# Kernel tuning notes

Hardware: AMD Instinct MI355X
Metric: run time of the kernel (lower is better)

Reference implementation:

```python
import jax, jax.numpy as jnp
import numpy as np

B, S, H = 4, 2048, 2048
E, K = 4, 2
FF = 4 * H  # standard MLP expert expansion


def setup_inputs() -> dict:
    key = jax.random.key(0)
    ks = jax.random.split(key, 5)
    sc = 0.02
    return {
        "hidden_states": jax.random.normal(ks[0], (B, S, H), jnp.float32),
        "w_gate": jax.random.normal(ks[1], (H, E), jnp.float32) * sc,
        "b_gate": jnp.zeros((E,), jnp.float32),
        "w1": jax.random.normal(ks[2], (E, H, FF), jnp.float32) * sc,
        "b1": jnp.zeros((E, FF), jnp.float32),
        "w2": jax.random.normal(ks[3], (E, FF, H), jnp.float32) * sc,
        "b2": jnp.zeros((E, H), jnp.float32),
    }


def reference(hidden_states, w_gate, b_gate, w1, b1, w2, b2):
    # Router: linear gate -> softmax -> top-k, renormalized gate weights
    logits = jnp.einsum("bsh,he->bse", hidden_states, w_gate) + b_gate
    probs = jax.nn.softmax(logits, axis=-1)                       # [B,S,E]
    top_p, top_i = jax.lax.top_k(probs, K)                        # [B,S,K]
    gate_w = top_p / jnp.sum(top_p, axis=-1, keepdims=True)

    # Switch-style load-balancing aux loss
    route = jax.nn.one_hot(top_i, E, dtype=probs.dtype)           # [B,S,K,E]
    frac_tokens = jnp.mean(jnp.sum(route, axis=2) / K, axis=(0, 1))  # [E]
    mean_prob = jnp.mean(probs, axis=(0, 1))                      # [E]
    aux_loss = E * jnp.sum(frac_tokens * mean_prob)

    # Dispatch/combine: small fixed expert count -> loop over experts,
    # dense FFN on all tokens, mask via gate weight (0 for unrouted tokens).
    out = jnp.zeros_like(hidden_states)
    for e in range(E):
        w_e = jnp.sum(gate_w * (top_i == e), axis=-1)             # [B,S]
        h = jax.nn.gelu(jnp.einsum("bsh,hf->bsf", hidden_states, w1[e]) + b1[e])
        y = jnp.einsum("bsf,fh->bsh", h, w2[e]) + b2[e]
        out = out + w_e[..., None] * y
    return out, aux_loss
```

## Files before the change

kernel.cpp:

```cpp
#include <hip/hip_runtime.h>

typedef unsigned short u16;
typedef __attribute__((ext_vector_type(8))) short bf16x8;
typedef __attribute__((ext_vector_type(4))) float f32x4;

#define TOK  8192
#define HD   2048
#define FFD  8192
#define NEXP 4
#define CAPE 4352

__device__ __forceinline__ u16 f2bf(float f){
  unsigned u = __float_as_uint(f);
  u += 0x7fffu + ((u >> 16) & 1u);
  return (u16)(u >> 16);
}

__device__ __forceinline__ float gelu_tanh(float x){
  float u = 0.7978845608028654f * (x + 0.044715f * x * x * x);
  return 0.5f * x * (1.0f + tanhf(u));
}

__device__ __forceinline__ void gload_lds16(const void* g, void* l){
  __builtin_amdgcn_global_load_lds((const __attribute__((address_space(1))) void*)g,
                                   (__attribute__((address_space(3))) void*)l, 16, 0, 0);
}

__device__ __forceinline__ f32x4 mfma_bf16(bf16x8 a, bf16x8 b, f32x4 c){
  asm("v_mfma_f32_16x16x32_bf16 %0, %1, %2, %0" : "+v"(c) : "v"(a), "v"(b));
  return c;
}

__global__ __launch_bounds__(256) void cvt_to_bf16(const float* __restrict__ in,
                                                   u16* __restrict__ out, int n4){
  int i = blockIdx.x * 256 + threadIdx.x;
  if (i >= n4) return;
  float4 v = ((const float4*)in)[i];
  ushort4 o;
  o.x = f2bf(v.x); o.y = f2bf(v.y); o.z = f2bf(v.z); o.w = f2bf(v.w);
  ((ushort4*)out)[i] = o;
}

__global__ __launch_bounds__(256) void transpose_cvt(const float* __restrict__ in,
                                                     u16* __restrict__ out, int R, int C){
  __shared__ u16 t[64][138];
  in  += (size_t)blockIdx.z * R * C;
  out += (size_t)blockIdx.z * R * C;
  const int tx = threadIdx.x & 63;
  const int w  = threadIdx.x >> 6;
  const size_t r0 = (size_t)blockIdx.y * 128;
  const size_t c0 = (size_t)blockIdx.x * 64;
  #pragma unroll
  for (int i = 0; i < 32; i++){
    const int r = w * 32 + i;
    t[tx][r] = f2bf(in[(r0 + r) * C + c0 + tx]);
  }
  __syncthreads();
  #pragma unroll
  for (int j = 0; j < 16; j++){
    const int c = j * 4 + w;
    ushort2 o;
    o.x = t[c][2 * tx];
    o.y = t[c][2 * tx + 1];
    *(ushort2*)(out + (c0 + c) * (size_t)R + r0 + 2 * tx) = o;
  }
}

__global__ __launch_bounds__(256) void router_kernel(
    const float* __restrict__ X, const float* __restrict__ wg, const float* __restrict__ bg,
    float* __restrict__ probs, int* __restrict__ topi, float* __restrict__ gatew){
  int t = blockIdx.x;
  const float* x = X + (size_t)t * HD;
  float a0 = 0.f, a1 = 0.f, a2 = 0.f, a3 = 0.f;
  for (int h = threadIdx.x; h < HD; h += 256){
    float xv = x[h];
    float4 w = ((const float4*)wg)[h];
    a0 += xv * w.x; a1 += xv * w.y; a2 += xv * w.z; a3 += xv * w.w;
  }
  __shared__ float red[4][256];
  red[0][threadIdx.x] = a0; red[1][threadIdx.x] = a1;
  red[2][threadIdx.x] = a2; red[3][threadIdx.x] = a3;
  __syncthreads();
  for (int s = 128; s > 0; s >>= 1){
    if (threadIdx.x < (unsigned)s){
      #pragma unroll
      for (int e = 0; e < 4; e++) red[e][threadIdx.x] += red[e][threadIdx.x + s];
    }
    __syncthreads();
  }
  if (threadIdx.x == 0){
    float l[4], p[4];
    #pragma unroll
    for (int e = 0; e < 4; e++) l[e] = red[e][0] + bg[e];
    float mx = fmaxf(fmaxf(l[0], l[1]), fmaxf(l[2], l[3]));
    float s = 0.f;
    #pragma unroll
    for (int e = 0; e < 4; e++){ p[e] = expf(l[e] - mx); s += p[e]; }
    #pragma unroll
    for (int e = 0; e < 4; e++){ p[e] /= s; probs[t * 4 + e] = p[e]; }
    int e0 = 0;
    for (int e = 1; e < 4; e++) if (p[e] > p[e0]) e0 = e;
    int e1 = -1;
    for (int e = 0; e < 4; e++){ if (e == e0) continue; if (e1 < 0 || p[e] > p[e1]) e1 = e; }
    float g = p[e0] + p[e1];
    topi[t * 2] = e0; topi[t * 2 + 1] = e1;
    #pragma unroll
    for (int e = 0; e < 4; e++)
      gatew[(size_t)e * TOK + t] = (e == e0) ? p[e0] / g : (e == e1) ? p[e1] / g : 0.f;
  }
}

__global__ __launch_bounds__(256) void compact_stage(const int* __restrict__ topi,
                                                     int* __restrict__ stage,
                                                     int* __restrict__ cnum){
  const int c = blockIdx.x, tid = threadIdx.x;
  const int t = c * 256 + tid;
  const int lane = tid & 63, w = tid >> 6;
  const int e0 = topi[t * 2], e1 = topi[t * 2 + 1];
  __shared__ int wcnt[4][4], woff[4][4];
  int pos[4]; bool sel[4];
  #pragma unroll
  for (int e = 0; e < 4; e++){
    sel[e] = (e0 == e) || (e1 == e);
    unsigned long long m = __ballot(sel[e]);
    pos[e] = __popcll(m & ((1ull << lane) - 1ull));
    if (lane == 0) wcnt[e][w] = __popcll(m);
  }
  __syncthreads();
  if (tid < 4){
    int s = 0;
    #pragma unroll
    for (int ww = 0; ww < 4; ww++){ woff[tid][ww] = s; s += wcnt[tid][ww]; }
    cnum[tid * 32 + c] = s;
  }
  __syncthreads();
  #pragma unroll
  for (int e = 0; e < 4; e++)
    if (sel[e]) stage[(e * 32 + c) * 256 + woff[e][w] + pos[e]] = t;
}

__global__ __launch_bounds__(64) void scan_chunks(const int* __restrict__ cnum,
                                                  int* __restrict__ coff,
                                                  int* __restrict__ cnt){
  if (threadIdx.x < 4){
    int e = threadIdx.x, s = 0;
    for (int c = 0; c < 32; c++){ coff[e * 32 + c] = s; s += cnum[e * 32 + c]; }
    cnt[e] = s;
  }
}

__global__ __launch_bounds__(256) void compact_write(const int* __restrict__ stage,
                                                     const int* __restrict__ cnum,
                                                     const int* __restrict__ coff,
                                                     int* __restrict__ lists){
  const int c = blockIdx.x, tid = threadIdx.x;
  #pragma unroll
  for (int e = 0; e < 4; e++){
    const int n = cnum[e * 32 + c];
    if (tid < n)
      lists[e * TOK + coff[e * 32 + c] + tid] = stage[(e * 32 + c) * 256 + tid];
  }
}

__global__ __launch_bounds__(256) void aux_kernel(const float* __restrict__ probs,
                                                  const int* __restrict__ topi,
                                                  float* __restrict__ out_aux){
  __shared__ float sp[4][256];
  __shared__ float sc[4][256];
  float p[4] = {0,0,0,0}, c[4] = {0,0,0,0};
  for (int t = threadIdx.x; t < TOK; t += 256){
    #pragma unroll
    for (int e = 0; e < 4; e++) p[e] += probs[t * 4 + e];
    c[topi[t * 2]]     += 1.f;
    c[topi[t * 2 + 1]] += 1.f;
  }
  #pragma unroll
  for (int e = 0; e < 4; e++){ sp[e][threadIdx.x] = p[e]; sc[e][threadIdx.x] = c[e]; }
  __syncthreads();
  for (int s = 128; s > 0; s >>= 1){
    if (threadIdx.x < (unsigned)s){
      #pragma unroll
      for (int e = 0; e < 4; e++){
        sp[e][threadIdx.x] += sp[e][threadIdx.x + s];
        sc[e][threadIdx.x] += sc[e][threadIdx.x + s];
      }
    }
    __syncthreads();
  }
  if (threadIdx.x == 0){
    float aux = 0.f;
    #pragma unroll
    for (int e = 0; e < 4; e++)
      aux += (sc[e][0] / (float)(TOK * 2)) * (sp[e][0] / (float)TOK);
    *out_aux = 4.f * aux;
  }
}

__global__ __launch_bounds__(256) void gemm1_97(
    const u16* __restrict__ Xb, const u16* __restrict__ BT,
    const int* __restrict__ lists, const int* __restrict__ cnt,
    const float* __restrict__ bias, u16* __restrict__ Hout)
{
  __shared__ __align__(16) u16 As[128 * 64];
  __shared__ __align__(16) u16 Bs[128 * 64];
  const int e = blockIdx.z;
  const int Mv = cnt[e];
  const int* rowidx = lists + (size_t)e * TOK;
  BT   += (size_t)e * (size_t)FFD * HD;
  bias += (size_t)e * FFD;
  Hout += (size_t)e * (size_t)CAPE * FFD;

  const int gx = gridDim.x, gy = gridDim.y;
  const int orig = blockIdx.x + gx * blockIdx.y;
  const int xcd = orig & 7, rank = orig >> 3;
  const int bxl = rank / gy, by = rank % gy;
  const int bx = xcd * (gx >> 3) + bxl;
  const int browg = by * 128;
  if (browg >= Mv) return;
  const size_t bcol = (size_t)bx * 128;

  const int tid = threadIdx.x, lane = tid & 63, w = tid >> 6;
  const int wr = w >> 1, wc = w & 1;
  const int l8 = lane >> 3;
  const int csw  = ((lane & 7) ^ l8) * 8;
  const int sw   = (lane & 7) * 8;
  const int h8   = ((lane >> 4) & 3) * 8;
  const int colk0 = h8 ^ sw, colk1 = (32 + h8) ^ sw;
  const int r16 = lane & 15;

  const u16* bsrc[4]; int bch[4];
  #pragma unroll
  for (int j = 0; j < 4; j++){
    int rb = j * 32 + w * 8;
    bch[j] = rb * 128;
    bsrc[j] = BT + (bcol + rb + l8) * (size_t)HD + csw;
  }
  const u16* asrc[4]; int ach[4];
  #pragma unroll
  for (int q = 0; q < 4; q++){
    int rb = wr * 64 + q * 16 + wc * 8;
    ach[q] = rb * 128;
    int rl = browg + rb + l8;
    if (rl > Mv - 1) rl = Mv - 1;
    asrc[q] = Xb + (size_t)rowidx[rl] * HD + csw;
  }

  f32x4 acc[4][4];
  #pragma unroll
  for (int m = 0; m < 4; m++)
    #pragma unroll
    for (int n = 0; n < 4; n++) acc[m][n] = (f32x4){0.f, 0.f, 0.f, 0.f};
  bf16x8 bC[8];

  const int NT = HD / 64;
  for (int t = 0; t < NT; ++t){
    const size_t ko = (size_t)t * 64;
    __syncthreads();
    #pragma unroll
    for (int j = 0; j < 4; j++) gload_lds16(bsrc[j] + ko, (char*)Bs + bch[j]);
    #pragma unroll
    for (int q = 0; q < 4; q++) gload_lds16(asrc[q] + ko, (char*)As + ach[q]);
    __syncthreads();

    #pragma unroll
    for (int nf = 0; nf < 4; nf++){
      const u16* bp = Bs + (wc * 64 + nf * 16 + r16) * 64;
      bC[nf * 2]     = *(const bf16x8*)(bp + colk0);
      bC[nf * 2 + 1] = *(const bf16x8*)(bp + colk1);
    }
    #pragma unroll
    for (int m = 0; m < 4; m++){
      const u16* ap = As + (wr * 64 + m * 16 + r16) * 64;
      bf16x8 a0 = *(const bf16x8*)(ap + colk0);
      bf16x8 a1 = *(const bf16x8*)(ap + colk1);
      #pragma unroll
      for (int nf = 0; nf < 4; nf++){
        acc[m][nf] = mfma_bf16(a0, bC[nf * 2],     acc[m][nf]);
        acc[m][nf] = mfma_bf16(a1, bC[nf * 2 + 1], acc[m][nf]);
      }
    }
  }

  const int cl = r16, rg = (lane >> 4) * 4;
  const size_t c0 = bcol + wc * 64;
  float bv[4];
  #pragma unroll
  for (int nf = 0; nf < 4; nf++) bv[nf] = bias[c0 + nf * 16 + cl];
  #pragma unroll
  for (int mf = 0; mf < 4; mf++){
    const int rbase = browg + wr * 64 + mf * 16 + rg;
    #pragma unroll
    for (int nf = 0; nf < 4; nf++){
      const size_t col = c0 + nf * 16 + cl;
      #pragma unroll
      for (int j = 0; j < 4; j++){
        u16 hv = f2bf(gelu_tanh(acc[mf][nf][j] + bv[nf]));
        __builtin_nontemporal_store(hv, &Hout[(size_t)(rbase + j) * FFD + col]);
      }
    }
  }
}

template<int ATOMIC>
__global__ __launch_bounds__(512) void gemm2_97(
    const u16* __restrict__ Hb, const u16* __restrict__ BT,
    const int* __restrict__ lists, const int* __restrict__ cnt,
    const float* __restrict__ bias, const float* __restrict__ gate,
    float* __restrict__ Cout)
{
  __shared__ __align__(16) u16 As[256 * 64];
  __shared__ __align__(16) u16 Bs[128 * 64];
  const int e = blockIdx.z;
  const int Mv = cnt[e];
  const int* rowidx = lists + (size_t)e * TOK;
  BT   += (size_t)e * (size_t)HD * FFD;
  bias += (size_t)e * HD;
  Hb   += (size_t)e * (size_t)CAPE * FFD;
  gate += (size_t)e * TOK;

  const int gx = gridDim.x, gy = gridDim.y;
  const int nwg = gx * gy;
  const int orig = blockIdx.x + gx * blockIdx.y;
  const int xcd = orig & 7, rank = orig >> 3;
  const int v = xcd * (nwg >> 3) + rank;
  const int bx = v % gx, by = v / gx;
  const int browg = by * 256;
  if (browg >= Mv) return;
  const size_t bcol = (size_t)bx * 128;

  const int tid = threadIdx.x, lane = tid & 63, w = tid >> 6;
  const int wm = w >> 1, wn = w & 1;
  const int l8 = lane >> 3;
  const int csw  = ((lane & 7) ^ l8) * 8;
  const int sw   = (lane & 7) * 8;
  const int h8   = ((lane >> 4) & 3) * 8;
  const int colk0 = h8 ^ sw, colk1 = (32 + h8) ^ sw;
  const int r16 = lane & 15;

  const u16* bsrc[2]; int bch[2];
  #pragma unroll
  for (int j = 0; j < 2; j++){
    int rb = j * 64 + w * 8;
    bch[j] = rb * 128;
    bsrc[j] = BT + (bcol + rb + l8) * (size_t)FFD + csw;
  }
  const u16* asrc[4]; int ach[4];
  #pragma unroll
  for (int q = 0; q < 4; q++){
    int rb = q * 64 + w * 8;
    ach[q] = rb * 128;
    asrc[q] = Hb + (size_t)(browg + rb + l8) * FFD + csw;
  }

  f32x4 acc[4][4];
  #pragma unroll
  for (int m = 0; m < 4; m++)
    #pragma unroll
    for (int n = 0; n < 4; n++) acc[m][n] = (f32x4){0.f, 0.f, 0.f, 0.f};
  bf16x8 bC[8];

  const int NT = FFD / 64;
  for (int t = 0; t < NT; ++t){
    const size_t ko = (size_t)t * 64;
    __syncthreads();
    #pragma unroll
    for (int j = 0; j < 2; j++) gload_lds16(bsrc[j] + ko, (char*)Bs + bch[j]);
    #pragma unroll
    for (int q = 0; q < 4; q++) gload_lds16(asrc[q] + ko, (char*)As + ach[q]);
    __syncthreads();

    #pragma unroll
    for (int nf = 0; nf < 4; nf++){
      const u16* bp = Bs + (wn * 64 + nf * 16 + r16) * 64;
      bC[nf * 2]     = *(const bf16x8*)(bp + colk0);
      bC[nf * 2 + 1] = *(const bf16x8*)(bp + colk1);
    }
    #pragma unroll
    for (int m = 0; m < 4; m++){
      const u16* ap = As + (wm * 64 + m * 16 + r16) * 64;
      bf16x8 a0 = *(const bf16x8*)(ap + colk0);
      bf16x8 a1 = *(const bf16x8*)(ap + colk1);
      #pragma unroll
      for (int nf = 0; nf < 4; nf++){
        acc[m][nf] = mfma_bf16(a0, bC[nf * 2],     acc[m][nf]);
        acc[m][nf] = mfma_bf16(a1, bC[nf * 2 + 1], acc[m][nf]);
      }
    }
  }

  const int cl = r16, rg = (lane >> 4) * 4;
  const size_t c0 = bcol + wn * 64;
  float bv[4];
  #pragma unroll
  for (int nf = 0; nf < 4; nf++) bv[nf] = bias[c0 + nf * 16 + cl];
  #pragma unroll
  for (int mf = 0; mf < 4; mf++){
    const int rbase = browg + wm * 64 + mf * 16 + rg;
    int   tok[4]; float gv[4];
    #pragma unroll
    for (int j = 0; j < 4; j++){
      const bool ok = (rbase + j) < Mv;
      tok[j] = ok ? rowidx[rbase + j] : -1;
      gv[j]  = ok ? gate[tok[j]] : 0.f;
    }
    #pragma unroll
    for (int nf = 0; nf < 4; nf++){
      const size_t col = c0 + nf * 16 + cl;
      #pragma unroll
      for (int j = 0; j < 4; j++){
        if (tok[j] >= 0){
          const size_t idx = (size_t)tok[j] * HD + col;
          float y = gv[j] * (acc[mf][nf][j] + bv[nf]);
          if (ATOMIC) atomicAdd(Cout + idx, y);
          else        Cout[idx] += y;
        }
      }
    }
  }
}

extern "C" void kernel_launch(void* const* d_in, const int* in_sizes, int n_in,
                              void* d_out, int out_size, void* d_ws, size_t ws_size,
                              hipStream_t stream){
  (void)in_sizes; (void)n_in;
  const float* X  = (const float*)d_in[0];
  const float* wg = (const float*)d_in[1];
  const float* bg = (const float*)d_in[2];
  const float* w1 = (const float*)d_in[3];
  const float* b1 = (const float*)d_in[4];
  const float* w2 = (const float*)d_in[5];
  const float* b2 = (const float*)d_in[6];
  float* out = (float*)d_out;

  char* ws = (char*)d_ws;
  size_t off = 0;
  auto alloc = [&](size_t b) -> char* {
    char* p = ws + off;
    off = (off + b + 255) & ~(size_t)255;
    return p;
  };
  u16*   Xb    = (u16*)  alloc((size_t)TOK * HD * 2);
  float* probs = (float*)alloc((size_t)TOK * 4 * 4);
  int*   topi  = (int*)  alloc((size_t)TOK * 2 * 4);
  float* gatew = (float*)alloc((size_t)NEXP * TOK * 4);
  int*   cnt   = (int*)  alloc((size_t)NEXP * 4);
  int*   lists = (int*)  alloc((size_t)NEXP * TOK * 4);
  int*   stage = (int*)  alloc((size_t)NEXP * 32 * 256 * 4);
  int*   cnum  = (int*)  alloc((size_t)NEXP * 32 * 4);
  int*   coff  = (int*)  alloc((size_t)NEXP * 32 * 4);
  const size_t common = off;

  const size_t w1t_all = (size_t)NEXP * FFD * HD * 2;
  const size_t w2t_all = (size_t)NEXP * HD * FFD * 2;
  const size_t hb_all  = (size_t)NEXP * CAPE * FFD * 2;
  const bool merged = ws_size >= common + w1t_all + w2t_all + hb_all + 1024;

  hipMemsetAsync(out, 0, (size_t)TOK * HD * sizeof(float), stream);

  cvt_to_bf16<<<(TOK * HD / 4 + 255) / 256, 256, 0, stream>>>(X, Xb, TOK * HD / 4);
  router_kernel<<<TOK, 256, 0, stream>>>(X, wg, bg, probs, topi, gatew);
  compact_stage<<<32, 256, 0, stream>>>(topi, stage, cnum);
  scan_chunks<<<1, 64, 0, stream>>>(cnum, coff, cnt);
  compact_write<<<32, 256, 0, stream>>>(stage, cnum, coff, lists);
  aux_kernel<<<1, 256, 0, stream>>>(probs, topi, out + (out_size - 1));

  if (merged){
    u16* W1T = (u16*)alloc(w1t_all);
    u16* W2T = (u16*)alloc(w2t_all);
    u16* Hb  = (u16*)alloc(hb_all);
    transpose_cvt<<<dim3(FFD / 64, HD / 128, NEXP), 256, 0, stream>>>(w1, W1T, HD, FFD);
    transpose_cvt<<<dim3(HD / 64, FFD / 128, NEXP), 256, 0, stream>>>(w2, W2T, FFD, HD);
    gemm1_97<<<dim3(FFD / 128, CAPE / 128, NEXP), 256, 0, stream>>>(
        Xb, W1T, lists, cnt, b1, Hb);
    gemm2_97<1><<<dim3(HD / 128, CAPE / 256, NEXP), 512, 0, stream>>>(
        Hb, W2T, lists, cnt, b2, gatew, out);
  } else {
    u16* W1T = (u16*)alloc((size_t)FFD * HD * 2);
    u16* W2T = (u16*)alloc((size_t)HD * FFD * 2);
    u16* Hb  = (u16*)alloc((size_t)CAPE * FFD * 2);
    for (int e = 0; e < NEXP; ++e){
      transpose_cvt<<<dim3(FFD / 64, HD / 128, 1), 256, 0, stream>>>(
          w1 + (size_t)e * HD * FFD, W1T, HD, FFD);
      transpose_cvt<<<dim3(HD / 64, FFD / 128, 1), 256, 0, stream>>>(
          w2 + (size_t)e * FFD * HD, W2T, FFD, HD);
      gemm1_97<<<dim3(FFD / 128, CAPE / 128, 1), 256, 0, stream>>>(
          Xb, W1T, lists + e * TOK, cnt + e, b1 + (size_t)e * FFD, Hb);
      gemm2_97<0><<<dim3(HD / 128, CAPE / 256, 1), 512, 0, stream>>>(
          Hb, W2T, lists + e * TOK, cnt + e, b2 + (size_t)e * HD,
          gatew + (size_t)e * TOK, out);
    }
  }
}
```

Before: 1.664 ms.

## Pipeline gemm1 with 256x256 double-buffered tiles and fuse bf16 cast into router

Replaces the first expert GEMM with a 512-thread 256x256 tile kernel. It double-buffers LDS and interleaves async global-to-LDS loads with MFMA phases, using explicit vmcnt waits, raw barriers and wave priority hints, so memory latency hides behind compute and the tile gets more reuse. The standalone X-to-bf16 conversion kernel is folded into the router, which already reads X, saving one full pass over the activations. The second GEMM changes from 256-row tiles with 512 threads to 128-row tiles with 256 threads, giving more, smaller blocks. This adds complex hand-scheduled synchronisation and register pressure, and a 256-row tile pads more rows per expert.

```diff
diff --git a/kernel.cpp b/kernel.cpp
--- a/kernel.cpp
+++ b/kernel.cpp
@@ -10,6 +10,9 @@
 #define NEXP 4
 #define CAPE 4352
 
+#define S_BARRIER() asm volatile("s_barrier" ::: "memory")
+#define VMCNT(n)    asm volatile("s_waitcnt vmcnt(" #n ")" ::: "memory")
+
 __device__ __forceinline__ u16 f2bf(float f){
   unsigned u = __float_as_uint(f);
   u += 0x7fffu + ((u >> 16) & 1u);
@@ -29,16 +32,6 @@
 __device__ __forceinline__ f32x4 mfma_bf16(bf16x8 a, bf16x8 b, f32x4 c){
   asm("v_mfma_f32_16x16x32_bf16 %0, %1, %2, %0" : "+v"(c) : "v"(a), "v"(b));
   return c;
-}
-
-__global__ __launch_bounds__(256) void cvt_to_bf16(const float* __restrict__ in,
-                                                   u16* __restrict__ out, int n4){
-  int i = blockIdx.x * 256 + threadIdx.x;
-  if (i >= n4) return;
-  float4 v = ((const float4*)in)[i];
-  ushort4 o;
-  o.x = f2bf(v.x); o.y = f2bf(v.y); o.z = f2bf(v.z); o.w = f2bf(v.w);
-  ((ushort4*)out)[i] = o;
 }
 
 __global__ __launch_bounds__(256) void transpose_cvt(const float* __restrict__ in,
@@ -68,14 +61,26 @@
 
 __global__ __launch_bounds__(256) void router_kernel(
     const float* __restrict__ X, const float* __restrict__ wg, const float* __restrict__ bg,
-    float* __restrict__ probs, int* __restrict__ topi, float* __restrict__ gatew){
+    float* __restrict__ probs, int* __restrict__ topi, float* __restrict__ gatew,
+    u16* __restrict__ Xb){
   int t = blockIdx.x;
-  const float* x = X + (size_t)t * HD;
+  const float4* x4  = (const float4*)(X + (size_t)t * HD);
+  ushort4*      xb4 = (ushort4*)(Xb + (size_t)t * HD);
+  const float4* wg4 = (const float4*)wg;
   float a0 = 0.f, a1 = 0.f, a2 = 0.f, a3 = 0.f;
-  for (int h = threadIdx.x; h < HD; h += 256){
-    float xv = x[h];
-    float4 w = ((const float4*)wg)[h];
-    a0 += xv * w.x; a1 += xv * w.y; a2 += xv * w.z; a3 += xv * w.w;
+  #pragma unroll
+  for (int it = 0; it < HD / 4 / 256; ++it){
+    const int h4 = it * 256 + threadIdx.x;
+    float4 xv = x4[h4];
+    ushort4 o;
+    o.x = f2bf(xv.x); o.y = f2bf(xv.y); o.z = f2bf(xv.z); o.w = f2bf(xv.w);
+    xb4[h4] = o;
+    float xe[4] = {xv.x, xv.y, xv.z, xv.w};
+    #pragma unroll
+    for (int j = 0; j < 4; j++){
+      float4 w = wg4[h4 * 4 + j];
+      a0 += xe[j] * w.x; a1 += xe[j] * w.y; a2 += xe[j] * w.z; a3 += xe[j] * w.w;
+    }
   }
   __shared__ float red[4][256];
   red[0][threadIdx.x] = a0; red[1][threadIdx.x] = a1;
@@ -196,19 +201,193 @@
   }
 }
 
-__global__ __launch_bounds__(256) void gemm1_97(
+__global__ __launch_bounds__(512, 2) void gemm1_8p(
     const u16* __restrict__ Xb, const u16* __restrict__ BT,
     const int* __restrict__ lists, const int* __restrict__ cnt,
     const float* __restrict__ bias, u16* __restrict__ Hout)
+{
+  __shared__ __align__(16) u16 As[2 * 256 * 64];
+  __shared__ __align__(16) u16 Bs[2 * 256 * 64];
+  const int e = blockIdx.z;
+  const int Mv = cnt[e];
+  const int* rowidx = lists + (size_t)e * TOK;
+  BT   += (size_t)e * (size_t)FFD * HD;
+  bias += (size_t)e * FFD;
+  Hout += (size_t)e * (size_t)CAPE * FFD;
+
+  const int gx = gridDim.x, gy = gridDim.y;
+  const int orig = blockIdx.x + gx * blockIdx.y;
+  const int xcd = orig & 7, rank = orig >> 3;
+  const int bxl = rank / gy, by = rank % gy;
+  const int bx = xcd * (gx >> 3) + bxl;
+  const int browg = by * 256;
+  if (browg >= Mv) return;
+  const size_t bcol = (size_t)bx * 256;
+
+  const int tid = threadIdx.x, lane = tid & 63, w = tid >> 6;
+  const int wm = w >> 2, wn = w & 3;
+  const int l8 = lane >> 3;
+  const int csw = ((lane & 7) ^ l8) * 8;
+  const int sw  = (lane & 7) * 8;
+  const int h8  = ((lane >> 4) & 3) * 8;
+  const int colk0 = h8 ^ sw, colk1 = (32 + h8) ^ sw;
+  const int r16 = lane & 15;
+
+  const u16* bsrc[4]; const u16* asrc[4]; int uch[4];
+  #pragma unroll
+  for (int i = 0; i < 4; i++){
+    const int rb = i * 64 + w * 8;
+    uch[i] = rb * 128;
+    bsrc[i] = BT + (bcol + rb + l8) * (size_t)HD + csw;
+    int rl = browg + rb + l8; if (rl > Mv - 1) rl = Mv - 1;
+    asrc[i] = Xb + (size_t)rowidx[rl] * HD + csw;
+  }
+
+  f32x4 acc[8][4];
+  #pragma unroll
+  for (int m = 0; m < 8; m++)
+    #pragma unroll
+    for (int n = 0; n < 4; n++) acc[m][n] = (f32x4){0.f, 0.f, 0.f, 0.f};
+  bf16x8 bC[8];
+
+  char* A0b = (char*)As;            char* A1b = (char*)As + 32768;
+  char* B0b = (char*)Bs;            char* B1b = (char*)Bs + 32768;
+  const u16* Ac0 = As;              const u16* Ac1 = As + 16384;
+  const u16* Bc0 = Bs;              const u16* Bc1 = Bs + 16384;
+
+  const int NT = HD / 64;
+
+  #pragma unroll
+  for (int j = 0; j < 4; j++) gload_lds16(bsrc[j], B0b + uch[j]);
+  #pragma unroll
+  for (int q = 0; q < 4; q++) gload_lds16(asrc[q], A0b + uch[q]);
+  #pragma unroll
+  for (int j = 0; j < 4; j++) gload_lds16(bsrc[j] + 64, B1b + uch[j]);
+  gload_lds16(asrc[0] + 64, A1b + uch[0]);
+  gload_lds16(asrc[2] + 64, A1b + uch[2]);
+  VMCNT(6); S_BARRIER();
+
+#define READ_A(Ac, m0)                                                     \
+  bf16x8 a[2][2];                                                          \
+  _Pragma("unroll")                                                        \
+  for (int mi = 0; mi < 2; mi++){                                          \
+    const u16* ap = (Ac) + (wm * 128 + ((m0) + mi) * 16 + r16) * 64;       \
+    a[mi][0] = *(const bf16x8*)(ap + colk0);                               \
+    a[mi][1] = *(const bf16x8*)(ap + colk1);                               \
+  }
+
+#define READ_B(Bc)                                                         \
+  _Pragma("unroll")                                                        \
+  for (int nf = 0; nf < 4; nf++){                                          \
+    const u16* bp = (Bc) + (wn * 64 + nf * 16 + r16) * 64;                 \
+    bC[nf * 2]     = *(const bf16x8*)(bp + colk0);                         \
+    bC[nf * 2 + 1] = *(const bf16x8*)(bp + colk1);                         \
+  }
+
+#define DO_MFMA(m0)                                                        \
+  __builtin_amdgcn_s_setprio(1);                                           \
+  _Pragma("unroll")                                                        \
+  for (int mi = 0; mi < 2; mi++)                                           \
+    _Pragma("unroll")                                                      \
+    for (int nf = 0; nf < 4; nf++){                                        \
+      acc[(m0) + mi][nf] = mfma_bf16(a[mi][0], bC[nf * 2],     acc[(m0) + mi][nf]); \
+      acc[(m0) + mi][nf] = mfma_bf16(a[mi][1], bC[nf * 2 + 1], acc[(m0) + mi][nf]); \
+    }                                                                      \
+  __builtin_amdgcn_s_setprio(0);
+
+  for (int it = 0; it < NT / 2; ++it){
+    const size_t k1 = (size_t)(2 * it + 1) * 64;
+    const size_t k2 = (size_t)(2 * it + 2) * 64;
+    const size_t k3 = (size_t)(2 * it + 3) * 64;
+    const bool s2 = (2 * it + 2 < NT);
+    const bool s3 = (2 * it + 3 < NT);
+
+    {
+      READ_B(Bc0); READ_A(Ac0, 0);
+      gload_lds16(asrc[1] + k1, A1b + uch[1]);
+      gload_lds16(asrc[3] + k1, A1b + uch[3]);
+      S_BARRIER(); DO_MFMA(0); S_BARRIER();
+    }
+    {
+      READ_A(Ac0, 2);
+      if (s2){ gload_lds16(bsrc[0] + k2, B0b + uch[0]); gload_lds16(bsrc[1] + k2, B0b + uch[1]); }
+      S_BARRIER(); DO_MFMA(2); S_BARRIER();
+    }
+    {
+      READ_A(Ac0, 4);
+      if (s2){ gload_lds16(bsrc[2] + k2, B0b + uch[2]); gload_lds16(bsrc[3] + k2, B0b + uch[3]); }
+      S_BARRIER(); DO_MFMA(4); S_BARRIER();
+    }
+    {
+      READ_A(Ac0, 6);
+      if (s2){ gload_lds16(asrc[0] + k2, A0b + uch[0]); gload_lds16(asrc[2] + k2, A0b + uch[2]); }
+      S_BARRIER(); DO_MFMA(6);
+      if (s2) VMCNT(6); else VMCNT(0);
+      S_BARRIER();
+    }
+    {
+      READ_B(Bc1); READ_A(Ac1, 0);
+      if (s2){ gload_lds16(asrc[1] + k2, A0b + uch[1]); gload_lds16(asrc[3] + k2, A0b + uch[3]); }
+      S_BARRIER(); DO_MFMA(0); S_BARRIER();
+    }
+    {
+      READ_A(Ac1, 2);
+      if (s3){ gload_lds16(bsrc[0] + k3, B1b + uch[0]); gload_lds16(bsrc[1] + k3, B1b + uch[1]); }
+      S_BARRIER(); DO_MFMA(2); S_BARRIER();
+    }
+    {
+      READ_A(Ac1, 4);
+      if (s3){ gload_lds16(bsrc[2] + k3, B1b + uch[2]); gload_lds16(bsrc[3] + k3, B1b + uch[3]); }
+      S_BARRIER(); DO_MFMA(4); S_BARRIER();
+    }
+    {
+      READ_A(Ac1, 6);
+      if (s3){ gload_lds16(asrc[0] + k3, A1b + uch[0]); gload_lds16(asrc[2] + k3, A1b + uch[2]); }
+      S_BARRIER(); DO_MFMA(6);
+      if (s3) VMCNT(6); else if (s2) VMCNT(0);
+      S_BARRIER();
+    }
+  }
+#undef READ_A
+#undef READ_B
+#undef DO_MFMA
+
+  const int cl = r16, rg = (lane >> 4) * 4;
+  const size_t c0 = bcol + wn * 64;
+  float bv[4];
+  #pragma unroll
+  for (int nf = 0; nf < 4; nf++) bv[nf] = bias[c0 + nf * 16 + cl];
+  #pragma unroll
+  for (int mf = 0; mf < 8; mf++){
+    const size_t rb = (size_t)(browg + wm * 128 + mf * 16 + rg);
+    #pragma unroll
+    for (int nf = 0; nf < 4; nf++){
+      const size_t col = c0 + nf * 16 + cl;
+      #pragma unroll
+      for (int j = 0; j < 4; j++){
+        u16 hv = f2bf(gelu_tanh(acc[mf][nf][j] + bv[nf]));
+        __builtin_nontemporal_store(hv, &Hout[(rb + j) * FFD + col]);
+      }
+    }
+  }
+}
+
+template<int ATOMIC>
+__global__ __launch_bounds__(256) void gemm2_97(
+    const u16* __restrict__ Hb, const u16* __restrict__ BT,
+    const int* __restrict__ lists, const int* __restrict__ cnt,
+    const float* __restrict__ bias, const float* __restrict__ gate,
+    float* __restrict__ Cout)
 {
   __shared__ __align__(16) u16 As[128 * 64];
   __shared__ __align__(16) u16 Bs[128 * 64];
   const int e = blockIdx.z;
   const int Mv = cnt[e];
   const int* rowidx = lists + (size_t)e * TOK;
-  BT   += (size_t)e * (size_t)FFD * HD;
-  bias += (size_t)e * FFD;
-  Hout += (size_t)e * (size_t)CAPE * FFD;
+  BT   += (size_t)e * (size_t)HD * FFD;
+  bias += (size_t)e * HD;
+  Hb   += (size_t)e * (size_t)CAPE * FFD;
+  gate += (size_t)e * TOK;
 
   const int gx = gridDim.x, gy = gridDim.y;
   const int orig = blockIdx.x + gx * blockIdx.y;
@@ -233,16 +412,14 @@
   for (int j = 0; j < 4; j++){
     int rb = j * 32 + w * 8;
     bch[j] = rb * 128;
-    bsrc[j] = BT + (bcol + rb + l8) * (size_t)HD + csw;
+    bsrc[j] = BT + (bcol + rb + l8) * (size_t)FFD + csw;
   }
   const u16* asrc[4]; int ach[4];
   #pragma unroll
   for (int q = 0; q < 4; q++){
     int rb = wr * 64 + q * 16 + wc * 8;
     ach[q] = rb * 128;
-    int rl = browg + rb + l8;
-    if (rl > Mv - 1) rl = Mv - 1;
-    asrc[q] = Xb + (size_t)rowidx[rl] * HD + csw;
+    asrc[q] = Hb + (size_t)(browg + rb + l8) * FFD + csw;
   }
 
   f32x4 acc[4][4];
@@ -252,7 +429,7 @@
     for (int n = 0; n < 4; n++) acc[m][n] = (f32x4){0.f, 0.f, 0.f, 0.f};
   bf16x8 bC[8];
 
-  const int NT = HD / 64;
+  const int NT = FFD / 64;
   for (int t = 0; t < NT; ++t){
     const size_t ko = (size_t)t * 64;
     __syncthreads();
@@ -289,113 +466,6 @@
   #pragma unroll
   for (int mf = 0; mf < 4; mf++){
     const int rbase = browg + wr * 64 + mf * 16 + rg;
-    #pragma unroll
-    for (int nf = 0; nf < 4; nf++){
-      const size_t col = c0 + nf * 16 + cl;
-      #pragma unroll
-      for (int j = 0; j < 4; j++){
-        u16 hv = f2bf(gelu_tanh(acc[mf][nf][j] + bv[nf]));
-        __builtin_nontemporal_store(hv, &Hout[(size_t)(rbase + j) * FFD + col]);
-      }
-    }
-  }
-}
-
-template<int ATOMIC>
-__global__ __launch_bounds__(512) void gemm2_97(
-    const u16* __restrict__ Hb, const u16* __restrict__ BT,
-    const int* __restrict__ lists, const int* __restrict__ cnt,
-    const float* __restrict__ bias, const float* __restrict__ gate,
-    float* __restrict__ Cout)
-{
-  __shared__ __align__(16) u16 As[256 * 64];
-  __shared__ __align__(16) u16 Bs[128 * 64];
-  const int e = blockIdx.z;
-  const int Mv = cnt[e];
-  const int* rowidx = lists + (size_t)e * TOK;
-  BT   += (size_t)e * (size_t)HD * FFD;
-  bias += (size_t)e * HD;
-  Hb   += (size_t)e * (size_t)CAPE * FFD;
-  gate += (size_t)e * TOK;
-
-  const int gx = gridDim.x, gy = gridDim.y;
-  const int nwg = gx * gy;
-  const int orig = blockIdx.x + gx * blockIdx.y;
-  const int xcd = orig & 7, rank = orig >> 3;
-  const int v = xcd * (nwg >> 3) + rank;
-  const int bx = v % gx, by = v / gx;
-  const int browg = by * 256;
-  if (browg >= Mv) return;
-  const size_t bcol = (size_t)bx * 128;
-
-  const int tid = threadIdx.x, lane = tid & 63, w = tid >> 6;
-  const int wm = w >> 1, wn = w & 1;
-  const int l8 = lane >> 3;
-  const int csw  = ((lane & 7) ^ l8) * 8;
-  const int sw   = (lane & 7) * 8;
-  const int h8   = ((lane >> 4) & 3) * 8;
-  const int colk0 = h8 ^ sw, colk1 = (32 + h8) ^ sw;
-  const int r16 = lane & 15;
-
-  const u16* bsrc[2]; int bch[2];
-  #pragma unroll
-  for (int j = 0; j < 2; j++){
-    int rb = j * 64 + w * 8;
-    bch[j] = rb * 128;
-    bsrc[j] = BT + (bcol + rb + l8) * (size_t)FFD + csw;
-  }
-  const u16* asrc[4]; int ach[4];
-  #pragma unroll
-  for (int q = 0; q < 4; q++){
-    int rb = q * 64 + w * 8;
-    ach[q] = rb * 128;
-    asrc[q] = Hb + (size_t)(browg + rb + l8) * FFD + csw;
-  }
-
-  f32x4 acc[4][4];
-  #pragma unroll
-  for (int m = 0; m < 4; m++)
-    #pragma unroll
-    for (int n = 0; n < 4; n++) acc[m][n] = (f32x4){0.f, 0.f, 0.f, 0.f};
-  bf16x8 bC[8];
-
-  const int NT = FFD / 64;
-  for (int t = 0; t < NT; ++t){
-    const size_t ko = (size_t)t * 64;
-    __syncthreads();
-    #pragma unroll
-    for (int j = 0; j < 2; j++) gload_lds16(bsrc[j] + ko, (char*)Bs + bch[j]);
-    #pragma unroll
-    for (int q = 0; q < 4; q++) gload_lds16(asrc[q] + ko, (char*)As + ach[q]);
-    __syncthreads();
-
-    #pragma unroll
-    for (int nf = 0; nf < 4; nf++){
-      const u16* bp = Bs + (wn * 64 + nf * 16 + r16) * 64;
-      bC[nf * 2]     = *(const bf16x8*)(bp + colk0);
-      bC[nf * 2 + 1] = *(const bf16x8*)(bp + colk1);
-    }
-    #pragma unroll
-    for (int m = 0; m < 4; m++){
-      const u16* ap = As + (wm * 64 + m * 16 + r16) * 64;
-      bf16x8 a0 = *(const bf16x8*)(ap + colk0);
-      bf16x8 a1 = *(const bf16x8*)(ap + colk1);
-      #pragma unroll
-      for (int nf = 0; nf < 4; nf++){
-        acc[m][nf] = mfma_bf16(a0, bC[nf * 2],     acc[m][nf]);
-        acc[m][nf] = mfma_bf16(a1, bC[nf * 2 + 1], acc[m][nf]);
-      }
-    }
-  }
-
-  const int cl = r16, rg = (lane >> 4) * 4;
-  const size_t c0 = bcol + wn * 64;
-  float bv[4];
-  #pragma unroll
-  for (int nf = 0; nf < 4; nf++) bv[nf] = bias[c0 + nf * 16 + cl];
-  #pragma unroll
-  for (int mf = 0; mf < 4; mf++){
-    const int rbase = browg + wm * 64 + mf * 16 + rg;
     int   tok[4]; float gv[4];
     #pragma unroll
     for (int j = 0; j < 4; j++){
@@ -457,8 +527,7 @@
 
   hipMemsetAsync(out, 0, (size_t)TOK * HD * sizeof(float), stream);
 
-  cvt_to_bf16<<<(TOK * HD / 4 + 255) / 256, 256, 0, stream>>>(X, Xb, TOK * HD / 4);
-  router_kernel<<<TOK, 256, 0, stream>>>(X, wg, bg, probs, topi, gatew);
+  router_kernel<<<TOK, 256, 0, stream>>>(X, wg, bg, probs, topi, gatew, Xb);
   compact_stage<<<32, 256, 0, stream>>>(topi, stage, cnum);
   scan_chunks<<<1, 64, 0, stream>>>(cnum, coff, cnt);
   compact_write<<<32, 256, 0, stream>>>(stage, cnum, coff, lists);
@@ -470,9 +539,9 @@
     u16* Hb  = (u16*)alloc(hb_all);
     transpose_cvt<<<dim3(FFD / 64, HD / 128, NEXP), 256, 0, stream>>>(w1, W1T, HD, FFD);
     transpose_cvt<<<dim3(HD / 64, FFD / 128, NEXP), 256, 0, stream>>>(w2, W2T, FFD, HD);
-    gemm1_97<<<dim3(FFD / 128, CAPE / 128, NEXP), 256, 0, stream>>>(
+    gemm1_8p<<<dim3(FFD / 256, CAPE / 256, NEXP), 512, 0, stream>>>(
         Xb, W1T, lists, cnt, b1, Hb);
-    gemm2_97<1><<<dim3(HD / 128, CAPE / 256, NEXP), 512, 0, stream>>>(
+    gemm2_97<1><<<dim3(HD / 128, CAPE / 128, NEXP), 256, 0, stream>>>(
         Hb, W2T, lists, cnt, b2, gatew, out);
   } else {
     u16* W1T = (u16*)alloc((size_t)FFD * HD * 2);
@@ -483,9 +552,9 @@
           w1 + (size_t)e * HD * FFD, W1T, HD, FFD);
       transpose_cvt<<<dim3(HD / 64, FFD / 128, 1), 256, 0, stream>>>(
           w2 + (size_t)e * FFD * HD, W2T, FFD, HD);
-      gemm1_97<<<dim3(FFD / 128, CAPE / 128, 1), 256, 0, stream>>>(
+      gemm1_8p<<<dim3(FFD / 256, CAPE / 256, 1), 512, 0, stream>>>(
           Xb, W1T, lists + e * TOK, cnt + e, b1 + (size_t)e * FFD, Hb);
-      gemm2_97<0><<<dim3(HD / 128, CAPE / 256, 1), 512, 0, stream>>>(
+      gemm2_97<0><<<dim3(HD / 128, CAPE / 128, 1), 256, 0, stream>>>(
           Hb, W2T, lists + e * TOK, cnt + e, b2 + (size_t)e * HD,
           gatew + (size_t)e * TOK, out);
     }
```

Measured after the change: 1.808 ms. 8.7% more time.
